# Kernel optimization log

Hardware: AMD Instinct MI355X
Metric: run time of the kernel (lower is better)

## Reference

```python
import jax, jax.numpy as jnp
import numpy as np

BS, HIST, H, W, NOBJ = 512, 3, 10, 10, 4
NSENT, TOK, DM = 3, 36, 768
EMB, FM, K, NL, ADIM = 256, 64, 2, 128, 5
LIN = FM * (H - (K - 1)) * (W - (K - 1))  # 64*9*9 = 5184
ATTN_SCALE = float(np.sqrt(EMB))  # 16.0


def setup_inputs() -> dict:
    key = jax.random.key(0)
    ks = jax.random.split(key, 24)
    g = lambda i, shape, s=0.02: jax.random.normal(ks[i], shape, dtype=jnp.float32) * s
    sprite_emb = g(0, (25, EMB), 1.0).at[0].set(0.0)  # padding_idx=0 -> zero row
    inp = {
        'state': jax.random.randint(ks[1], (BS, HIST, H, W, NOBJ), 0, 25, dtype=jnp.int32),
        'action': jax.random.randint(ks[2], (BS,), 0, ADIM, dtype=jnp.int32),
        'temb': jax.random.normal(ks[3], (BS, NSENT, TOK, DM), dtype=jnp.float32),
        'sprite_emb': sprite_emb,
        'conv_w': g(4, (K, K, HIST * EMB, FM)),  # HWIO
        'conv_b': g(5, (FM,)),
        'Wk': g(6, (DM, EMB)), 'bk': g(7, (EMB,)),
        'Wks': g(8, (DM, 1)), 'bks': g(9, (1,)),
        'Wv': g(10, (DM, EMB)), 'bv': g(11, (EMB,)),
        'Wvs': g(12, (DM, 1)), 'bvs': g(13, (1,)),
        'a1': g(14, (LIN, NL)), 'a1b': g(15, (NL,)),
        'a2': g(16, (NL, NL)), 'a2b': g(17, (NL,)),
        'a3': g(18, (NL, ADIM)), 'a3b': g(19, (ADIM,)),
        'v1': g(20, (LIN, NL)), 'v1b': g(21, (NL,)),
        'v2': g(22, (NL, NL)), 'v2b': g(23, (NL,)),
        'v3': jax.random.normal(jax.random.fold_in(key, 99), (NL, 1)) * 0.02,
        'v3b': jnp.zeros((1,), jnp.float32),
    }
    return inp


def _nonzero_mean(e):
    # e: [..., n, emb]; mean over rows that are nonzero (padding rows are all-zero)
    cnt = jnp.sum(jnp.sum(e, axis=-1) != 0, axis=-1, keepdims=True)
    return jnp.sum(e, axis=-2) / jnp.maximum(cnt, 1).astype(e.dtype)


def reference(state, action, temb, sprite_emb, conv_w, conv_b, Wk, bk, Wks, bks,
              Wv, bv, Wvs, bvs, a1, a1b, a2, a2b, a3, a3b, v1, v1b, v2, v2b, v3, v3b):
    lrelu = jax.nn.leaky_relu  # slope 0.01 matches torch default
    bs = state.shape[0]
    obj_state, avt_state = state[..., :-1], state[..., -1:]
    query = _nonzero_mean(sprite_emb[obj_state])   # [bs,hist,H,W,emb]
    avatar = _nonzero_mean(sprite_emb[avt_state])  # [bs,hist,H,W,emb]
    # text key/value: scaled token-softmax pooling over tokens (dim=2)
    k = (temb @ Wk + bk) * jax.nn.softmax(temb @ Wks + bks, axis=-2)
    k = jnp.sum(k, axis=2)                          # [bs,nsent,emb]
    v = (temb @ Wv + bv) * jax.nn.softmax(temb @ Wvs + bvs, axis=-2)
    v = jnp.sum(v, axis=2)                          # [bs,nsent,emb]
    # batch_attention
    q2 = query.reshape(bs, -1, EMB)                 # [bs, hist*H*W, emb]
    kq = jnp.einsum('bxe,bse->bxs', q2, k) / ATTN_SCALE
    wts = jax.nn.softmax(kq, axis=-1) * (kq != 0)
    wts = wts.reshape(bs, HIST, H, W, NSENT)
    # mean(weights[...,None]*value, dim=-2) == (w @ v) / nsent
    att = jnp.einsum('bthws,bse->bthwe', wts, v) / NSENT  # [bs,hist,H,W,emb]
    st = att.reshape(bs, H, W, -1)                  # fold hist into channels (768)
    av = avatar.reshape(bs, H, W, -1)
    st = (st + av) / 2.0                            # NHWC, C=768
    y = jax.lax.conv_general_dilated(st, conv_w, (1, 1), 'VALID',
                                     dimension_numbers=('NHWC', 'HWIO', 'NHWC')) + conv_b
    y = lrelu(y)                                    # [bs,9,9,64]
    y = jnp.transpose(y, (0, 3, 1, 2)).reshape(bs, -1)  # torch NCHW flatten order
    ha = lrelu(lrelu(y @ a1 + a1b) @ a2 + a2b)
    logits = ha @ a3 + a3b
    logp = jax.nn.log_softmax(logits, axis=-1)
    action_logprobs = jnp.take_along_axis(logp, action[:, None].astype(jnp.int32), axis=-1)[:, 0]
    entropy = -jnp.sum(jnp.exp(logp) * logp, axis=-1)
    hv = lrelu(lrelu(y @ v1 + v1b) @ v2 + v2b)
    state_value = (hv @ v3 + v3b)[:, 0]
    return action_logprobs, state_value, entropy
```

## Files before the change

kernel.cpp:

```cpp
#include <hip/hip_runtime.h>
#include <hip/hip_bf16.h>
#include <math.h>

constexpr int BS   = 512;
constexpr int NBS  = 1536;
constexpr int NPOS = 300;
constexpr int LIN  = 5184;
constexpr int KSPLIT = 9, KCH = 576;

typedef __attribute__((ext_vector_type(8))) short bf16x8;
typedef __attribute__((ext_vector_type(4))) float f32x4;

static __device__ __forceinline__ short f2bf(float f) {
    unsigned u = __float_as_uint(f);
    unsigned r = (u + 0x7FFFu + ((u >> 16) & 1u)) >> 16;
    return (short)r;
}
static __device__ __forceinline__ unsigned pk2(float a, float b) {
    return ((unsigned)(unsigned short)f2bf(a)) | (((unsigned)(unsigned short)f2bf(b)) << 16);
}
static __device__ __forceinline__ float bf2f_lo(unsigned u) { return __uint_as_float(u << 16); }
static __device__ __forceinline__ float bf2f_hi(unsigned u) { return __uint_as_float(u & 0xFFFF0000u); }

constexpr size_t OFF_RD   = 0;
constexpr size_t OFF_FL   = 19968;
constexpr size_t OFF_DT   = 20032;
constexpr size_t OFF_WCT  = 118336;
constexpr size_t OFF_PH   = 413248;
constexpr size_t OFF_AB   = 437824;
constexpr size_t OFF_SK   = 1101376;
constexpr size_t OFF_SV   = 1156672;
constexpr size_t OFF_SWK  = 1211968;
constexpr size_t OFF_SWV  = 1267264;
constexpr size_t OFF_XKH  = 1322560;
constexpr size_t OFF_XVH  = 1912384;
constexpr size_t OFF_VWH  = 2502208;
constexpr size_t OFF_YH   = 3092032;
constexpr size_t OFF_PART = 4419136;

__global__ __launch_bounds__(256) void kS_scores_prep(
    const float* __restrict__ temb, const float* __restrict__ Wks,
    const float* __restrict__ Wvs, const float* __restrict__ conv_w,
    const float* __restrict__ sprite, const float* __restrict__ Wk,
    const float* __restrict__ Wv, const float* __restrict__ bv,
    const float* __restrict__ a1, const float* __restrict__ v1,
    float* __restrict__ SK, float* __restrict__ SV,
    short* __restrict__ AB, short* __restrict__ PH, short* __restrict__ WCT,
    float* __restrict__ RD, int* __restrict__ FL)
{
    __shared__ float tile[64][65];
    int tid = threadIdx.x, bx = blockIdx.x;

    if (bx < 13824) {
        int wid = tid >> 6, lane = tid & 63;
        size_t r = (size_t)bx * 4 + wid;
        const float4* row = (const float4*)temb + r * 192;
        const float4* k4 = (const float4*)Wks;
        const float4* v4 = (const float4*)Wvs;
        float pk = 0.f, pv = 0.f;
        #pragma unroll
        for (int i = 0; i < 3; ++i) {
            int d4 = lane + 64 * i;
            float4 x = row[d4];
            float4 wk = k4[d4], wv = v4[d4];
            pk += x.x * wk.x + x.y * wk.y + x.z * wk.z + x.w * wk.w;
            pv += x.x * wv.x + x.y * wv.y + x.z * wv.z + x.w * wv.w;
        }
        #pragma unroll
        for (int off = 32; off; off >>= 1) {
            pk += __shfl_down(pk, off);
            pv += __shfl_down(pv, off);
        }
        if (lane == 0) { SK[r] = pk; SV[r] = pv; }
        return;
    }

    int id = bx - 13824;
    if (id < 324) {
        int kt = id % 81, nt = id / 81;
        const float* src = (nt < 2) ? a1 : v1;
        int col0 = (nt & 1) * 64;
        #pragma unroll
        for (int it = 0; it < 16; ++it) {
            int idx = it * 256 + tid; int ki = idx >> 6, ni = idx & 63;
            tile[ki][ni] = src[(size_t)(kt * 64 + ki) * 128 + col0 + ni];
        }
        __syncthreads();
        #pragma unroll
        for (int it = 0; it < 16; ++it) {
            int idx = it * 256 + tid; int ni = idx >> 6, ki = idx & 63;
            AB[(size_t)(nt * 64 + ni) * 5184 + kt * 64 + ki] = f2bf(tile[ki][ni]);
        }
    } else if (id < 399) {
        int g = (id - 324) * 256 + tid;
        if (g < 19200) {
            int o = g / 768, d = g - o * 768;
            const float* sp = sprite + o * 256;
            const float* wr = Wk + (size_t)d * 256;
            float s = 0.f;
            for (int c = 0; c < 256; ++c) s += sp[c] * wr[c];
            PH[(size_t)o * 768 + d] = f2bf(s);
        }
    } else if (id < 477) {
        int g = (id - 399) * 256 + tid;
        if (g < 19968) {
            int o = g / 768, n = g - o * 768;
            int tap = n >> 6, f = n & 63; int t4 = tap / 3, j = tap - t4 * 3;
            const float* sp = (o < 25) ? (sprite + o * 256) : bv;
            float s = 0.f;
            for (int e = 0; e < 256; ++e)
                s += sp[e] * conv_w[(size_t)(t4 * 768 + j * 256 + e) * 64 + f];
            RD[g] = s;
        }
    } else if (id < 621) {
        int wid2 = id - 477;
        int bm = (wid2 / 12) * 64, bn = (wid2 % 12) * 64;
        int p = bm >> 6; int t4 = p / 3, jj = p - t4 * 3;
        const float* cwb = conv_w + (size_t)(t4 * 768 + jj * 256) * 64;
        float* As = (float*)tile;
        float* Bs = (float*)tile + 2080;
        float acc[4][4];
        #pragma unroll
        for (int i = 0; i < 4; ++i)
            #pragma unroll
            for (int j = 0; j < 4; ++j) acc[i][j] = 0.f;
        int tm = tid >> 4, tn = tid & 15;
        for (int kc = 0; kc < 256; kc += 32) {
            #pragma unroll
            for (int it = 0; it < 8; ++it) {
                int idx = it * 256 + tid; int c = idx >> 6, f = idx & 63;
                As[c * 65 + f] = cwb[(size_t)(kc + c) * 64 + f];
            }
            #pragma unroll
            for (int it = 0; it < 8; ++it) {
                int idx = it * 256 + tid; int d = idx >> 5, c = idx & 31;
                Bs[c * 65 + d] = Wv[(size_t)(bn + d) * 256 + kc + c];
            }
            __syncthreads();
            for (int kk = 0; kk < 32; ++kk) {
                float a[4], b[4];
                #pragma unroll
                for (int i = 0; i < 4; ++i) a[i] = As[kk * 65 + tm * 4 + i];
                #pragma unroll
                for (int j = 0; j < 4; ++j) b[j] = Bs[kk * 65 + tn * 4 + j];
                #pragma unroll
                for (int i = 0; i < 4; ++i)
                    #pragma unroll
                    for (int j = 0; j < 4; ++j) acc[i][j] += a[i] * b[j];
            }
            __syncthreads();
        }
        #pragma unroll
        for (int i = 0; i < 4; ++i)
            #pragma unroll
            for (int j = 0; j < 4; ++j)
                WCT[(size_t)(bm + tm * 4 + i) * 768 + bn + tn * 4 + j] = f2bf(acc[i][j]);
    } else {
        if (tid < 25) {
            float s = 0.f;
            for (int c = 0; c < 256; ++c) s += sprite[tid * 256 + c];
            FL[tid] = (s != 0.0f) ? 1 : 0;
        }
    }
}

__global__ __launch_bounds__(512) void kW_weights(
    const float* __restrict__ SK, const float* __restrict__ SV,
    float* __restrict__ SWK, float* __restrict__ SWV)
{
    int w = threadIdx.x >> 6, lane = threadIdx.x & 63;
    int bs = blockIdx.x * 8 + w;
    {
        float s = (lane < 36) ? SK[(size_t)bs * 36 + lane] : -1e30f;
        float m = s;
        #pragma unroll
        for (int off = 32; off; off >>= 1) m = fmaxf(m, __shfl_xor(m, off));
        float e = (lane < 36) ? expf(s - m) : 0.f;
        float z = e;
        #pragma unroll
        for (int off = 32; off; off >>= 1) z += __shfl_xor(z, off);
        if (lane < 36) SWK[(size_t)bs * 36 + lane] = e / z;
    }
    {
        float s = (lane < 36) ? SV[(size_t)bs * 36 + lane] : -1e30f;
        float m = s;
        #pragma unroll
        for (int off = 32; off; off >>= 1) m = fmaxf(m, __shfl_xor(m, off));
        float e = (lane < 36) ? expf(s - m) : 0.f;
        float z = e;
        #pragma unroll
        for (int off = 32; off; off >>= 1) z += __shfl_xor(z, off);
        if (lane < 36) SWV[(size_t)bs * 36 + lane] = e / z;
    }
}

__global__ __launch_bounds__(192) void kX_sum(
    const float* __restrict__ temb, const float* __restrict__ SWK,
    const float* __restrict__ SWV, short* __restrict__ XKH, short* __restrict__ XVH)
{
    __shared__ float sw[72];
    int tid = threadIdx.x, bs = blockIdx.x;
    if (tid < 36) sw[tid] = SWK[(size_t)bs * 36 + tid];
    else if (tid >= 64 && tid < 100) sw[tid - 28] = SWV[(size_t)bs * 36 + tid - 64];
    __syncthreads();

    const float4* row4 = (const float4*)temb + (size_t)bs * 6912;
    float k0 = 0.f, k1 = 0.f, k2 = 0.f, k3 = 0.f;
    float v0 = 0.f, v1 = 0.f, v2 = 0.f, v3 = 0.f;
    #pragma unroll
    for (int b = 0; b < 3; ++b) {
        float4 xv[12];
        #pragma unroll
        for (int j = 0; j < 12; ++j) xv[j] = row4[(size_t)(b * 12 + j) * 192 + tid];
        #pragma unroll
        for (int j = 0; j < 12; ++j) {
            int t = b * 12 + j;
            float wk = sw[t], wv = sw[36 + t];
            k0 += wk * xv[j].x; k1 += wk * xv[j].y;
            k2 += wk * xv[j].z; k3 += wk * xv[j].w;
            v0 += wv * xv[j].x; v1 += wv * xv[j].y;
            v2 += wv * xv[j].z; v3 += wv * xv[j].w;
        }
    }
    uint2 hk = { pk2(k0, k1), pk2(k2, k3) };
    uint2 hv = { pk2(v0, v1), pk2(v2, v3) };
    ((uint2*)XKH)[(size_t)bs * 192 + tid] = hk;
    ((uint2*)XVH)[(size_t)bs * 192 + tid] = hv;
}

template<int BIAS, int OUTBF>
__global__ __launch_bounds__(256) void gemm_mfma(
    const short* __restrict__ A, const short* __restrict__ B,
    const float* __restrict__ bias, void* __restrict__ Cout,
    int K, int ldc, int klen, size_t czstride)
{
    __shared__ short As[64][40];
    __shared__ short Bs[64][40];
    int tid = threadIdx.x;
    int bm = blockIdx.x * 64, bn = blockIdx.y * 64;
    int wid = tid >> 6, lane = tid & 63;
    int wm = (wid >> 1) * 32, wn = (wid & 1) * 32;
    int l15 = lane & 15, lg = lane >> 4;

    f32x4 zero = {0.f, 0.f, 0.f, 0.f};
    f32x4 acc00 = zero, acc01 = zero, acc10 = zero, acc11 = zero;

    int srow = tid >> 2, kch = (tid & 3) * 8;
    const short* Ap = A + (size_t)(bm + srow) * K + kch + (size_t)blockIdx.z * klen;
    const short* Bp = B + (size_t)(bn + srow) * K + kch + (size_t)blockIdx.z * klen;

    for (int kt = 0; kt < klen; kt += 32) {
        bf16x8 aval = *(const bf16x8*)(Ap + kt);
        bf16x8 bval = *(const bf16x8*)(Bp + kt);
        *(bf16x8*)&As[srow][kch] = aval;
        *(bf16x8*)&Bs[srow][kch] = bval;
        __syncthreads();
        bf16x8 af0 = *(const bf16x8*)&As[wm + l15][lg * 8];
        bf16x8 af1 = *(const bf16x8*)&As[wm + 16 + l15][lg * 8];
        bf16x8 bg0 = *(const bf16x8*)&Bs[wn + l15][lg * 8];
        bf16x8 bg1 = *(const bf16x8*)&Bs[wn + 16 + l15][lg * 8];
        acc00 = __builtin_amdgcn_mfma_f32_16x16x32_bf16(af0, bg0, acc00, 0, 0, 0);
        acc01 = __builtin_amdgcn_mfma_f32_16x16x32_bf16(af0, bg1, acc01, 0, 0, 0);
        acc10 = __builtin_amdgcn_mfma_f32_16x16x32_bf16(af1, bg0, acc10, 0, 0, 0);
        acc11 = __builtin_amdgcn_mfma_f32_16x16x32_bf16(af1, bg1, acc11, 0, 0, 0);
        __syncthreads();
    }

    float* Cf = (float*)Cout + (size_t)blockIdx.z * czstride;
    short* Ch = (short*)Cout;
    #pragma unroll
    for (int i = 0; i < 2; ++i) {
        f32x4 arow0 = (i == 0) ? acc00 : acc10;
        f32x4 arow1 = (i == 0) ? acc01 : acc11;
        #pragma unroll
        for (int j = 0; j < 2; ++j) {
            f32x4 a = (j == 0) ? arow0 : arow1;
            int col = bn + wn + j * 16 + l15;
            float bb = BIAS ? bias[col] : 0.f;
            #pragma unroll
            for (int r = 0; r < 4; ++r) {
                int row = bm + wm + i * 16 + lg * 4 + r;
                float v = a[r] + bb;
                if (OUTBF) Ch[(size_t)row * ldc + col] = f2bf(v);
                else       Cf[(size_t)row * ldc + col] = v;
            }
        }
    }
}

__global__ __launch_bounds__(256) void k3_vwdt(
    const short* __restrict__ XVH, const short* __restrict__ WCT,
    const float* __restrict__ bvW2, short* __restrict__ VWH,
    const short* __restrict__ XKH, const short* __restrict__ PH,
    float* __restrict__ DT)
{
    __shared__ short As[64][40];
    __shared__ short Bs[64][40];
    int tid = threadIdx.x;
    bool isdt = (blockIdx.y == 12);
    const short* A = isdt ? XKH : XVH;
    const short* B = isdt ? PH  : WCT;
    int bm = blockIdx.x * 64, bn = isdt ? 0 : blockIdx.y * 64;
    int wid = tid >> 6, lane = tid & 63;
    int wm = (wid >> 1) * 32, wn = (wid & 1) * 32;
    int l15 = lane & 15, lg = lane >> 4;

    f32x4 zero = {0.f, 0.f, 0.f, 0.f};
    f32x4 acc00 = zero, acc01 = zero, acc10 = zero, acc11 = zero;

    int srow = tid >> 2, kch = (tid & 3) * 8;
    const short* Ap = A + (size_t)(bm + srow) * 768 + kch;
    const short* Bp = B + (size_t)(bn + srow) * 768 + kch;

    for (int kt = 0; kt < 768; kt += 32) {
        bf16x8 aval = *(const bf16x8*)(Ap + kt);
        bf16x8 bval = *(const bf16x8*)(Bp + kt);
        *(bf16x8*)&As[srow][kch] = aval;
        *(bf16x8*)&Bs[srow][kch] = bval;
        __syncthreads();
        bf16x8 af0 = *(const bf16x8*)&As[wm + l15][lg * 8];
        bf16x8 af1 = *(const bf16x8*)&As[wm + 16 + l15][lg * 8];
        bf16x8 bg0 = *(const bf16x8*)&Bs[wn + l15][lg * 8];
        bf16x8 bg1 = *(const bf16x8*)&Bs[wn + 16 + l15][lg * 8];
        acc00 = __builtin_amdgcn_mfma_f32_16x16x32_bf16(af0, bg0, acc00, 0, 0, 0);
        acc01 = __builtin_amdgcn_mfma_f32_16x16x32_bf16(af0, bg1, acc01, 0, 0, 0);
        acc10 = __builtin_amdgcn_mfma_f32_16x16x32_bf16(af1, bg0, acc10, 0, 0, 0);
        acc11 = __builtin_amdgcn_mfma_f32_16x16x32_bf16(af1, bg1, acc11, 0, 0, 0);
        __syncthreads();
    }

    #pragma unroll
    for (int i = 0; i < 2; ++i) {
        f32x4 arow0 = (i == 0) ? acc00 : acc10;
        f32x4 arow1 = (i == 0) ? acc01 : acc11;
        #pragma unroll
        for (int j = 0; j < 2; ++j) {
            f32x4 a = (j == 0) ? arow0 : arow1;
            int col = bn + wn + j * 16 + l15;
            #pragma unroll
            for (int r = 0; r < 4; ++r) {
                int row = bm + wm + i * 16 + lg * 4 + r;
                if (isdt) DT[(size_t)row * 64 + col] = a[r];
                else      VWH[(size_t)row * 768 + col] = f2bf(a[r] + bvW2[col]);
            }
        }
    }
}

__global__ __launch_bounds__(512) void k4_y(
    const int* __restrict__ state, const float* __restrict__ dt,
    const int* __restrict__ flags, const short* __restrict__ VWH,
    const float* __restrict__ rowdot, const float* __restrict__ conv_b,
    short* __restrict__ y)
{
    int b = blockIdx.x, tid = threadIdx.x;
    __shared__ float s_vW[3 * 768];
    __shared__ float s_w[3][NPOS + 4];
    __shared__ int   s_avt[NPOS + 4];
    __shared__ float s_y[81 * 65];

    const unsigned* vr = (const unsigned*)(VWH + (size_t)b * 3 * 768);
    for (int i = tid; i < 1152; i += 512) {
        unsigned u = vr[i];
        s_vW[2 * i]     = bf2f_lo(u);
        s_vW[2 * i + 1] = bf2f_hi(u);
    }

    for (int code = tid; code < NPOS; code += 512) {
        const int* st = state + ((size_t)b * NPOS + code) * 4;
        int o0 = st[0], o1 = st[1], o2 = st[2], avi = st[3];
        int cnt = flags[o0] + flags[o1] + flags[o2];
        s_avt[code] = avi;
        float w0 = 0.f, w1 = 0.f, w2 = 0.f;
        if (cnt > 0) {
            const float* d0 = dt + (size_t)b * 192;
            float inv = 1.0f / (16.0f * (float)cnt);
            float q0 = (d0[o0]       + d0[o1]       + d0[o2])       * inv;
            float q1 = (d0[64 + o0]  + d0[64 + o1]  + d0[64 + o2])  * inv;
            float q2 = (d0[128 + o0] + d0[128 + o1] + d0[128 + o2]) * inv;
            float m = fmaxf(q0, fmaxf(q1, q2));
            float e0 = expf(q0 - m), e1 = expf(q1 - m), e2 = expf(q2 - m);
            float is = 1.0f / (6.0f * (e0 + e1 + e2));
            w0 = e0 * is; w1 = e1 * is; w2 = e2 * is;
        }
        s_w[0][code] = w0; s_w[1][code] = w1; s_w[2][code] = w2;
    }
    __syncthreads();

    int f = tid & 63;
    float cb = conv_b[f];
    for (int p = tid >> 6; p < 81; p += 8) {
        int oh = p / 9, ow = p - oh * 9;
        float acc = cb;
        #pragma unroll
        for (int kh = 0; kh < 2; ++kh)
        #pragma unroll
        for (int kw = 0; kw < 2; ++kw) {
            int bc = 3 * ((oh + kh) * 10 + (ow + kw));
            int tbase = ((kh * 2 + kw) * 3) * 64 + f;
            #pragma unroll
            for (int j = 0; j < 3; ++j) {
                int code = bc + j;
                int tf = tbase + j * 64;
                acc += s_w[0][code] * s_vW[tf]
                     + s_w[1][code] * s_vW[768 + tf]
                     + s_w[2][code] * s_vW[2 * 768 + tf];
                acc += 0.5f * rowdot[(size_t)s_avt[code] * 768 + tf];
            }
        }
        acc = acc > 0.f ? acc : 0.01f * acc;
        s_y[p * 65 + f] = acc;
    }
    __syncthreads();
    for (int i = tid; i < LIN; i += 512) {
        int ff = i / 81, pp = i - ff * 81;
        y[(size_t)b * LIN + i] = f2bf(s_y[pp * 65 + ff]);
    }
}

__global__ __launch_bounds__(128) void k6_heads(
    const float* __restrict__ PART, const float* __restrict__ a1b,
    const float* __restrict__ v1b, const int* __restrict__ action,
    const float* __restrict__ a2, const float* __restrict__ a2b,
    const float* __restrict__ a3, const float* __restrict__ a3b,
    const float* __restrict__ v2, const float* __restrict__ v2b,
    const float* __restrict__ v3, const float* __restrict__ v3b,
    float* __restrict__ out)
{
    int b = blockIdx.x, tid = threadIdx.x;
    __shared__ float h1a[128], h1v[128], h2a[128], red[128];
    __shared__ float lg[5];
    float sa0 = a1b[tid], sv0 = v1b[tid];
    const float* pb = PART + (size_t)b * 256;
    for (int z = 0; z < KSPLIT; ++z) {
        sa0 += pb[(size_t)z * (BS * 256) + tid];
        sv0 += pb[(size_t)z * (BS * 256) + 128 + tid];
    }
    h1a[tid] = sa0 > 0.f ? sa0 : 0.01f * sa0;
    h1v[tid] = sv0 > 0.f ? sv0 : 0.01f * sv0;
    __syncthreads();
    float sa = a2b[tid], sv = v2b[tid];
    for (int k = 0; k < 128; ++k) {
        sa += h1a[k] * a2[k * 128 + tid];
        sv += h1v[k] * v2[k * 128 + tid];
    }
    sa = sa > 0.f ? sa : 0.01f * sa;
    sv = sv > 0.f ? sv : 0.01f * sv;
    h2a[tid] = sa;
    red[tid] = sv * v3[tid];
    __syncthreads();
    for (int s = 64; s > 0; s >>= 1) {
        if (tid < s) red[tid] += red[tid + s];
        __syncthreads();
    }
    if (tid < 5) {
        float l = a3b[tid];
        for (int k = 0; k < 128; ++k) l += h2a[k] * a3[k * 5 + tid];
        lg[tid] = l;
    }
    __syncthreads();
    if (tid == 0) {
        float m = lg[0];
        for (int j2 = 1; j2 < 5; ++j2) m = fmaxf(m, lg[j2]);
        float se = 0.f;
        for (int j2 = 0; j2 < 5; ++j2) se += expf(lg[j2] - m);
        float lse = m + logf(se);
        int act = action[b];
        float ent = 0.f;
        for (int j2 = 0; j2 < 5; ++j2) {
            float lp = lg[j2] - lse;
            ent -= expf(lp) * lp;
        }
        out[b]        = lg[act] - lse;
        out[512 + b]  = red[0] + v3b[0];
        out[1024 + b] = ent;
    }
}

extern "C" void kernel_launch(void* const* d_in, const int* in_sizes, int n_in,
                              void* d_out, int out_size, void* d_ws, size_t ws_size,
                              hipStream_t stream)
{
    const int*   state  = (const int*)d_in[0];
    const int*   action = (const int*)d_in[1];
    const float* temb   = (const float*)d_in[2];
    const float* sprite = (const float*)d_in[3];
    const float* conv_w = (const float*)d_in[4];
    const float* conv_b = (const float*)d_in[5];
    const float* Wk     = (const float*)d_in[6];
    const float* Wks    = (const float*)d_in[8];
    const float* Wv     = (const float*)d_in[10];
    const float* bv     = (const float*)d_in[11];
    const float* Wvs    = (const float*)d_in[12];
    const float* a1     = (const float*)d_in[14];
    const float* a1b    = (const float*)d_in[15];
    const float* a2     = (const float*)d_in[16];
    const float* a2b    = (const float*)d_in[17];
    const float* a3     = (const float*)d_in[18];
    const float* a3b    = (const float*)d_in[19];
    const float* v1     = (const float*)d_in[20];
    const float* v1b    = (const float*)d_in[21];
    const float* v2     = (const float*)d_in[22];
    const float* v2b    = (const float*)d_in[23];
    const float* v3     = (const float*)d_in[24];
    const float* v3b    = (const float*)d_in[25];
    (void)in_sizes; (void)n_in; (void)out_size; (void)ws_size;

    float* ws  = (float*)d_ws;
    float* RD  = ws + OFF_RD;
    float* bvW2= RD + 25 * 768;
    int*   FL  = (int*)(ws + OFF_FL);
    float* DT  = ws + OFF_DT;
    short* WCT = (short*)(ws + OFF_WCT);
    short* PH  = (short*)(ws + OFF_PH);
    short* AB  = (short*)(ws + OFF_AB);
    float* SK  = ws + OFF_SK;
    float* SV  = ws + OFF_SV;
    float* SWK = ws + OFF_SWK;
    float* SWV = ws + OFF_SWV;
    short* XKH = (short*)(ws + OFF_XKH);
    short* XVH = (short*)(ws + OFF_XVH);
    short* VWH = (short*)(ws + OFF_VWH);
    short* YH  = (short*)(ws + OFF_YH);
    float* PART= ws + OFF_PART;
    float* out = (float*)d_out;

    kS_scores_prep<<<13824 + 622, 256, 0, stream>>>(
        temb, Wks, Wvs, conv_w, sprite, Wk, Wv, bv, a1, v1,
        SK, SV, AB, PH, WCT, RD, FL);
    kW_weights<<<192, 512, 0, stream>>>(SK, SV, SWK, SWV);
    kX_sum<<<NBS, 192, 0, stream>>>(temb, SWK, SWV, XKH, XVH);
    k3_vwdt<<<dim3(24,13,1),256,0,stream>>>(XVH, WCT, bvW2, VWH, XKH, PH, DT);
    k4_y<<<BS, 512, 0, stream>>>(state, DT, FL, VWH, RD, conv_b, YH);
    gemm_mfma<0,0><<<dim3(8,4,KSPLIT),256,0,stream>>>(YH, AB, nullptr, PART, 5184, 256, KCH, (size_t)BS*256);
    k6_heads<<<BS, 128, 0, stream>>>(PART, a1b, v1b, action, a2, a2b, a3, a3b,
                                     v2, v2b, v3, v3b, out);
}
```

Before: 137.7 us.

## Fuse token scoring, softmax and weighted pooling into one temb pass

```diff
diff --git a/kernel.cpp b/kernel.cpp
--- a/kernel.cpp
+++ b/kernel.cpp
@@ -28,81 +28,162 @@
 constexpr size_t OFF_WCT  = 118336;
 constexpr size_t OFF_PH   = 413248;
 constexpr size_t OFF_AB   = 437824;
-constexpr size_t OFF_SK   = 1101376;
-constexpr size_t OFF_SV   = 1156672;
-constexpr size_t OFF_SWK  = 1211968;
-constexpr size_t OFF_SWV  = 1267264;
-constexpr size_t OFF_XKH  = 1322560;
-constexpr size_t OFF_XVH  = 1912384;
-constexpr size_t OFF_VWH  = 2502208;
-constexpr size_t OFF_YH   = 3092032;
-constexpr size_t OFF_PART = 4419136;
-
-__global__ __launch_bounds__(256) void kS_scores_prep(
+constexpr size_t OFF_XKH  = 1101376;
+constexpr size_t OFF_XVH  = 1691200;
+constexpr size_t OFF_VWH  = 2281024;
+constexpr size_t OFF_YH   = 2870848;
+constexpr size_t OFF_PART = 4197952;
+
+#define DOT4(a,b) ((a).x*(b).x + (a).y*(b).y + (a).z*(b).z + (a).w*(b).w)
+#define WRED(v) { v += __shfl_down(v,32); v += __shfl_down(v,16); v += __shfl_down(v,8); \
+                  v += __shfl_down(v,4);  v += __shfl_down(v,2);  v += __shfl_down(v,1); }
+
+__global__ __launch_bounds__(576) void kT_temb_prep(
     const float* __restrict__ temb, const float* __restrict__ Wks,
     const float* __restrict__ Wvs, const float* __restrict__ conv_w,
     const float* __restrict__ sprite, const float* __restrict__ Wk,
     const float* __restrict__ Wv, const float* __restrict__ bv,
     const float* __restrict__ a1, const float* __restrict__ v1,
-    float* __restrict__ SK, float* __restrict__ SV,
+    short* __restrict__ XKH, short* __restrict__ XVH,
     short* __restrict__ AB, short* __restrict__ PH, short* __restrict__ WCT,
     float* __restrict__ RD, int* __restrict__ FL)
 {
-    __shared__ float tile[64][65];
+    __shared__ float spart[9][26];
+    __shared__ float swt[80];
+    __shared__ float big[4608];
     int tid = threadIdx.x, bx = blockIdx.x;
 
-    if (bx < 13824) {
-        int wid = tid >> 6, lane = tid & 63;
-        size_t r = (size_t)bx * 4 + wid;
-        const float4* row = (const float4*)temb + r * 192;
-        const float4* k4 = (const float4*)Wks;
-        const float4* v4 = (const float4*)Wvs;
-        float pk = 0.f, pv = 0.f;
-        #pragma unroll
-        for (int i = 0; i < 3; ++i) {
-            int d4 = lane + 64 * i;
-            float4 x = row[d4];
-            float4 wk = k4[d4], wv = v4[d4];
-            pk += x.x * wk.x + x.y * wk.y + x.z * wk.z + x.w * wk.w;
-            pv += x.x * wv.x + x.y * wv.y + x.z * wv.z + x.w * wv.w;
-        }
-        #pragma unroll
-        for (int off = 32; off; off >>= 1) {
-            pk += __shfl_down(pk, off);
-            pv += __shfl_down(pv, off);
-        }
-        if (lane == 0) { SK[r] = pk; SV[r] = pv; }
+    if (bx < NBS) {
+        int bs = bx;
+        int w = tid >> 6, lane = tid & 63;
+        int g = tid / 192, c = tid - g * 192;
+        const float4* row4 = (const float4*)temb + (size_t)bs * 6912 + (size_t)g * 2304 + c;
+
+        float4 x0  = row4[0];
+        float4 x1  = row4[192];
+        float4 x2  = row4[384];
+        float4 x3  = row4[576];
+        float4 x4  = row4[768];
+        float4 x5  = row4[960];
+        float4 x6  = row4[1152];
+        float4 x7  = row4[1344];
+        float4 x8  = row4[1536];
+        float4 x9  = row4[1728];
+        float4 x10 = row4[1920];
+        float4 x11 = row4[2112];
+        float4 wk = ((const float4*)Wks)[c];
+        float4 wv = ((const float4*)Wvs)[c];
+
+        float pk0 = DOT4(x0,wk),  pv0 = DOT4(x0,wv);
+        float pk1 = DOT4(x1,wk),  pv1 = DOT4(x1,wv);
+        float pk2_ = DOT4(x2,wk), pv2 = DOT4(x2,wv);
+        float pk3 = DOT4(x3,wk),  pv3 = DOT4(x3,wv);
+        float pk4 = DOT4(x4,wk),  pv4 = DOT4(x4,wv);
+        float pk5 = DOT4(x5,wk),  pv5 = DOT4(x5,wv);
+        float pk6 = DOT4(x6,wk),  pv6 = DOT4(x6,wv);
+        float pk7 = DOT4(x7,wk),  pv7 = DOT4(x7,wv);
+        float pk8 = DOT4(x8,wk),  pv8 = DOT4(x8,wv);
+        float pk9 = DOT4(x9,wk),  pv9 = DOT4(x9,wv);
+        float pk10 = DOT4(x10,wk), pv10 = DOT4(x10,wv);
+        float pk11 = DOT4(x11,wk), pv11 = DOT4(x11,wv);
+
+        WRED(pk0)  WRED(pk1)  WRED(pk2_) WRED(pk3)  WRED(pk4)  WRED(pk5)
+        WRED(pk6)  WRED(pk7)  WRED(pk8)  WRED(pk9)  WRED(pk10) WRED(pk11)
+        WRED(pv0)  WRED(pv1)  WRED(pv2)  WRED(pv3)  WRED(pv4)  WRED(pv5)
+        WRED(pv6)  WRED(pv7)  WRED(pv8)  WRED(pv9)  WRED(pv10) WRED(pv11)
+
+        if (lane == 0) {
+            spart[w][0] = pk0;   spart[w][1] = pk1;   spart[w][2] = pk2_;
+            spart[w][3] = pk3;   spart[w][4] = pk4;   spart[w][5] = pk5;
+            spart[w][6] = pk6;   spart[w][7] = pk7;   spart[w][8] = pk8;
+            spart[w][9] = pk9;   spart[w][10] = pk10; spart[w][11] = pk11;
+            spart[w][12] = pv0;  spart[w][13] = pv1;  spart[w][14] = pv2;
+            spart[w][15] = pv3;  spart[w][16] = pv4;  spart[w][17] = pv5;
+            spart[w][18] = pv6;  spart[w][19] = pv7;  spart[w][20] = pv8;
+            spart[w][21] = pv9;  spart[w][22] = pv10; spart[w][23] = pv11;
+        }
+        __syncthreads();
+
+        if (w == 0) {
+            float sk = -INFINITY, sv = -INFINITY;
+            if (lane < 36) {
+                int t = lane, gg = t / 12, j = t - gg * 12;
+                sk = spart[3*gg][j]    + spart[3*gg+1][j]    + spart[3*gg+2][j];
+                sv = spart[3*gg][12+j] + spart[3*gg+1][12+j] + spart[3*gg+2][12+j];
+            }
+            float mk = sk, mv = sv;
+            #pragma unroll
+            for (int off = 32; off; off >>= 1) {
+                mk = fmaxf(mk, __shfl_xor(mk, off));
+                mv = fmaxf(mv, __shfl_xor(mv, off));
+            }
+            float ek = (lane < 36) ? expf(sk - mk) : 0.f;
+            float ev = (lane < 36) ? expf(sv - mv) : 0.f;
+            float zk = ek, zv = ev;
+            #pragma unroll
+            for (int off = 32; off; off >>= 1) {
+                zk += __shfl_xor(zk, off);
+                zv += __shfl_xor(zv, off);
+            }
+            if (lane < 36) { swt[lane] = ek / zk; swt[40 + lane] = ev / zv; }
+        }
+        __syncthreads();
+
+        float4 ak = {0.f,0.f,0.f,0.f}, av = {0.f,0.f,0.f,0.f};
+        int wb = 12 * g;
+        #define ACCJ(J, XJ) { float a_ = swt[wb + J], b_ = swt[40 + wb + J]; \
+            ak.x += a_*XJ.x; ak.y += a_*XJ.y; ak.z += a_*XJ.z; ak.w += a_*XJ.w; \
+            av.x += b_*XJ.x; av.y += b_*XJ.y; av.z += b_*XJ.z; av.w += b_*XJ.w; }
+        ACCJ(0,x0) ACCJ(1,x1) ACCJ(2,x2) ACCJ(3,x3) ACCJ(4,x4) ACCJ(5,x5)
+        ACCJ(6,x6) ACCJ(7,x7) ACCJ(8,x8) ACCJ(9,x9) ACCJ(10,x10) ACCJ(11,x11)
+        #undef ACCJ
+
+        float4* red = (float4*)big;
+        red[g * 192 + c] = ak;
+        red[576 + g * 192 + c] = av;
+        __syncthreads();
+        if (tid < 192) {
+            float4 a0 = red[tid], a1_ = red[192 + tid], a2 = red[384 + tid];
+            float4 b0 = red[576 + tid], b1 = red[768 + tid], b2 = red[960 + tid];
+            float kx = a0.x + a1_.x + a2.x, ky = a0.y + a1_.y + a2.y;
+            float kz = a0.z + a1_.z + a2.z, kw = a0.w + a1_.w + a2.w;
+            float vx = b0.x + b1.x + b2.x, vy = b0.y + b1.y + b2.y;
+            float vz = b0.z + b1.z + b2.z, vw = b0.w + b1.w + b2.w;
+            uint2 hk = { pk2(kx, ky), pk2(kz, kw) };
+            uint2 hv = { pk2(vx, vy), pk2(vz, vw) };
+            ((uint2*)XKH)[(size_t)bs * 192 + tid] = hk;
+            ((uint2*)XVH)[(size_t)bs * 192 + tid] = hv;
+        }
         return;
     }
 
-    int id = bx - 13824;
+    int id = bx - NBS;
     if (id < 324) {
+        float (*tile)[65] = (float(*)[65])big;
         int kt = id % 81, nt = id / 81;
         const float* src = (nt < 2) ? a1 : v1;
         int col0 = (nt & 1) * 64;
-        #pragma unroll
-        for (int it = 0; it < 16; ++it) {
-            int idx = it * 256 + tid; int ki = idx >> 6, ni = idx & 63;
+        for (int idx = tid; idx < 4096; idx += 576) {
+            int ki = idx >> 6, ni = idx & 63;
             tile[ki][ni] = src[(size_t)(kt * 64 + ki) * 128 + col0 + ni];
         }
         __syncthreads();
-        #pragma unroll
-        for (int it = 0; it < 16; ++it) {
-            int idx = it * 256 + tid; int ni = idx >> 6, ki = idx & 63;
+        for (int idx = tid; idx < 4096; idx += 576) {
+            int ni = idx >> 6, ki = idx & 63;
             AB[(size_t)(nt * 64 + ni) * 5184 + kt * 64 + ki] = f2bf(tile[ki][ni]);
         }
-    } else if (id < 399) {
-        int g = (id - 324) * 256 + tid;
+    } else if (id < 358) {
+        int g = (id - 324) * 576 + tid;
         if (g < 19200) {
             int o = g / 768, d = g - o * 768;
             const float* sp = sprite + o * 256;
             const float* wr = Wk + (size_t)d * 256;
             float s = 0.f;
-            for (int c = 0; c < 256; ++c) s += sp[c] * wr[c];
+            for (int cc = 0; cc < 256; ++cc) s += sp[cc] * wr[cc];
             PH[(size_t)o * 768 + d] = f2bf(s);
         }
-    } else if (id < 477) {
-        int g = (id - 399) * 256 + tid;
+    } else if (id < 393) {
+        int g = (id - 358) * 576 + tid;
         if (g < 19968) {
             int o = g / 768, n = g - o * 768;
             int tap = n >> 6, f = n & 63; int t4 = tap / 3, j = tap - t4 * 3;
@@ -112,178 +193,56 @@
                 s += sp[e] * conv_w[(size_t)(t4 * 768 + j * 256 + e) * 64 + f];
             RD[g] = s;
         }
-    } else if (id < 621) {
-        int wid2 = id - 477;
+    } else if (id < 537) {
+        int wid2 = id - 393;
         int bm = (wid2 / 12) * 64, bn = (wid2 % 12) * 64;
         int p = bm >> 6; int t4 = p / 3, jj = p - t4 * 3;
         const float* cwb = conv_w + (size_t)(t4 * 768 + jj * 256) * 64;
-        float* As = (float*)tile;
-        float* Bs = (float*)tile + 2080;
+        float* As = big;
+        float* Bs = big + 2080;
         float acc[4][4];
         #pragma unroll
         for (int i = 0; i < 4; ++i)
             #pragma unroll
             for (int j = 0; j < 4; ++j) acc[i][j] = 0.f;
-        int tm = tid >> 4, tn = tid & 15;
+        int tm = (tid & 255) >> 4, tn = tid & 15;
         for (int kc = 0; kc < 256; kc += 32) {
-            #pragma unroll
-            for (int it = 0; it < 8; ++it) {
-                int idx = it * 256 + tid; int c = idx >> 6, f = idx & 63;
-                As[c * 65 + f] = cwb[(size_t)(kc + c) * 64 + f];
-            }
-            #pragma unroll
-            for (int it = 0; it < 8; ++it) {
-                int idx = it * 256 + tid; int d = idx >> 5, c = idx & 31;
-                Bs[c * 65 + d] = Wv[(size_t)(bn + d) * 256 + kc + c];
+            for (int idx = tid; idx < 2048; idx += 576) {
+                int cc = idx >> 6, f = idx & 63;
+                As[cc * 65 + f] = cwb[(size_t)(kc + cc) * 64 + f];
+            }
+            for (int idx = tid; idx < 2048; idx += 576) {
+                int d = idx >> 5, cc = idx & 31;
+                Bs[cc * 65 + d] = Wv[(size_t)(bn + d) * 256 + kc + cc];
             }
             __syncthreads();
-            for (int kk = 0; kk < 32; ++kk) {
-                float a[4], b[4];
+            if (tid < 256) {
+                for (int kk = 0; kk < 32; ++kk) {
+                    float a[4], b[4];
+                    #pragma unroll
+                    for (int i = 0; i < 4; ++i) a[i] = As[kk * 65 + tm * 4 + i];
+                    #pragma unroll
+                    for (int j = 0; j < 4; ++j) b[j] = Bs[kk * 65 + tn * 4 + j];
+                    #pragma unroll
+                    for (int i = 0; i < 4; ++i)
+                        #pragma unroll
+                        for (int j = 0; j < 4; ++j) acc[i][j] += a[i] * b[j];
+                }
+            }
+            __syncthreads();
+        }
+        if (tid < 256) {
+            #pragma unroll
+            for (int i = 0; i < 4; ++i)
                 #pragma unroll
-                for (int i = 0; i < 4; ++i) a[i] = As[kk * 65 + tm * 4 + i];
-                #pragma unroll
-                for (int j = 0; j < 4; ++j) b[j] = Bs[kk * 65 + tn * 4 + j];
-                #pragma unroll
-                for (int i = 0; i < 4; ++i)
-                    #pragma unroll
-                    for (int j = 0; j < 4; ++j) acc[i][j] += a[i] * b[j];
-            }
-            __syncthreads();
-        }
-        #pragma unroll
-        for (int i = 0; i < 4; ++i)
-            #pragma unroll
-            for (int j = 0; j < 4; ++j)
-                WCT[(size_t)(bm + tm * 4 + i) * 768 + bn + tn * 4 + j] = f2bf(acc[i][j]);
+                for (int j = 0; j < 4; ++j)
+                    WCT[(size_t)(bm + tm * 4 + i) * 768 + bn + tn * 4 + j] = f2bf(acc[i][j]);
+        }
     } else {
         if (tid < 25) {
             float s = 0.f;
-            for (int c = 0; c < 256; ++c) s += sprite[tid * 256 + c];
+            for (int cc = 0; cc < 256; ++cc) s += sprite[tid * 256 + cc];
             FL[tid] = (s != 0.0f) ? 1 : 0;
-        }
-    }
-}
-
-__global__ __launch_bounds__(512) void kW_weights(
-    const float* __restrict__ SK, const float* __restrict__ SV,
-    float* __restrict__ SWK, float* __restrict__ SWV)
-{
-    int w = threadIdx.x >> 6, lane = threadIdx.x & 63;
-    int bs = blockIdx.x * 8 + w;
-    {
-        float s = (lane < 36) ? SK[(size_t)bs * 36 + lane] : -1e30f;
-        float m = s;
-        #pragma unroll
-        for (int off = 32; off; off >>= 1) m = fmaxf(m, __shfl_xor(m, off));
-        float e = (lane < 36) ? expf(s - m) : 0.f;
-        float z = e;
-        #pragma unroll
-        for (int off = 32; off; off >>= 1) z += __shfl_xor(z, off);
-        if (lane < 36) SWK[(size_t)bs * 36 + lane] = e / z;
-    }
-    {
-        float s = (lane < 36) ? SV[(size_t)bs * 36 + lane] : -1e30f;
-        float m = s;
-        #pragma unroll
-        for (int off = 32; off; off >>= 1) m = fmaxf(m, __shfl_xor(m, off));
-        float e = (lane < 36) ? expf(s - m) : 0.f;
-        float z = e;
-        #pragma unroll
-        for (int off = 32; off; off >>= 1) z += __shfl_xor(z, off);
-        if (lane < 36) SWV[(size_t)bs * 36 + lane] = e / z;
-    }
-}
-
-__global__ __launch_bounds__(192) void kX_sum(
-    const float* __restrict__ temb, const float* __restrict__ SWK,
-    const float* __restrict__ SWV, short* __restrict__ XKH, short* __restrict__ XVH)
-{
-    __shared__ float sw[72];
-    int tid = threadIdx.x, bs = blockIdx.x;
-    if (tid < 36) sw[tid] = SWK[(size_t)bs * 36 + tid];
-    else if (tid >= 64 && tid < 100) sw[tid - 28] = SWV[(size_t)bs * 36 + tid - 64];
-    __syncthreads();
-
-    const float4* row4 = (const float4*)temb + (size_t)bs * 6912;
-    float k0 = 0.f, k1 = 0.f, k2 = 0.f, k3 = 0.f;
-    float v0 = 0.f, v1 = 0.f, v2 = 0.f, v3 = 0.f;
-    #pragma unroll
-    for (int b = 0; b < 3; ++b) {
-        float4 xv[12];
-        #pragma unroll
-        for (int j = 0; j < 12; ++j) xv[j] = row4[(size_t)(b * 12 + j) * 192 + tid];
-        #pragma unroll
-        for (int j = 0; j < 12; ++j) {
-            int t = b * 12 + j;
-            float wk = sw[t], wv = sw[36 + t];
-            k0 += wk * xv[j].x; k1 += wk * xv[j].y;
-            k2 += wk * xv[j].z; k3 += wk * xv[j].w;
-            v0 += wv * xv[j].x; v1 += wv * xv[j].y;
-            v2 += wv * xv[j].z; v3 += wv * xv[j].w;
-        }
-    }
-    uint2 hk = { pk2(k0, k1), pk2(k2, k3) };
-    uint2 hv = { pk2(v0, v1), pk2(v2, v3) };
-    ((uint2*)XKH)[(size_t)bs * 192 + tid] = hk;
-    ((uint2*)XVH)[(size_t)bs * 192 + tid] = hv;
-}
-
-template<int BIAS, int OUTBF>
-__global__ __launch_bounds__(256) void gemm_mfma(
-    const short* __restrict__ A, const short* __restrict__ B,
-    const float* __restrict__ bias, void* __restrict__ Cout,
-    int K, int ldc, int klen, size_t czstride)
-{
-    __shared__ short As[64][40];
-    __shared__ short Bs[64][40];
-    int tid = threadIdx.x;
-    int bm = blockIdx.x * 64, bn = blockIdx.y * 64;
-    int wid = tid >> 6, lane = tid & 63;
-    int wm = (wid >> 1) * 32, wn = (wid & 1) * 32;
-    int l15 = lane & 15, lg = lane >> 4;
-
-    f32x4 zero = {0.f, 0.f, 0.f, 0.f};
-    f32x4 acc00 = zero, acc01 = zero, acc10 = zero, acc11 = zero;
-
-    int srow = tid >> 2, kch = (tid & 3) * 8;
-    const short* Ap = A + (size_t)(bm + srow) * K + kch + (size_t)blockIdx.z * klen;
-    const short* Bp = B + (size_t)(bn + srow) * K + kch + (size_t)blockIdx.z * klen;
-
-    for (int kt = 0; kt < klen; kt += 32) {
-        bf16x8 aval = *(const bf16x8*)(Ap + kt);
-        bf16x8 bval = *(const bf16x8*)(Bp + kt);
-        *(bf16x8*)&As[srow][kch] = aval;
-        *(bf16x8*)&Bs[srow][kch] = bval;
-        __syncthreads();
-        bf16x8 af0 = *(const bf16x8*)&As[wm + l15][lg * 8];
-        bf16x8 af1 = *(const bf16x8*)&As[wm + 16 + l15][lg * 8];
-        bf16x8 bg0 = *(const bf16x8*)&Bs[wn + l15][lg * 8];
-        bf16x8 bg1 = *(const bf16x8*)&Bs[wn + 16 + l15][lg * 8];
-        acc00 = __builtin_amdgcn_mfma_f32_16x16x32_bf16(af0, bg0, acc00, 0, 0, 0);
-        acc01 = __builtin_amdgcn_mfma_f32_16x16x32_bf16(af0, bg1, acc01, 0, 0, 0);
-        acc10 = __builtin_amdgcn_mfma_f32_16x16x32_bf16(af1, bg0, acc10, 0, 0, 0);
-        acc11 = __builtin_amdgcn_mfma_f32_16x16x32_bf16(af1, bg1, acc11, 0, 0, 0);
-        __syncthreads();
-    }
-
-    float* Cf = (float*)Cout + (size_t)blockIdx.z * czstride;
-    short* Ch = (short*)Cout;
-    #pragma unroll
-    for (int i = 0; i < 2; ++i) {
-        f32x4 arow0 = (i == 0) ? acc00 : acc10;
-        f32x4 arow1 = (i == 0) ? acc01 : acc11;
-        #pragma unroll
-        for (int j = 0; j < 2; ++j) {
-            f32x4 a = (j == 0) ? arow0 : arow1;
-            int col = bn + wn + j * 16 + l15;
-            float bb = BIAS ? bias[col] : 0.f;
-            #pragma unroll
-            for (int r = 0; r < 4; ++r) {
-                int row = bm + wm + i * 16 + lg * 4 + r;
-                float v = a[r] + bb;
-                if (OUTBF) Ch[(size_t)row * ldc + col] = f2bf(v);
-                else       Cf[(size_t)row * ldc + col] = v;
-            }
         }
     }
 }
@@ -342,6 +301,66 @@
                 int row = bm + wm + i * 16 + lg * 4 + r;
                 if (isdt) DT[(size_t)row * 64 + col] = a[r];
                 else      VWH[(size_t)row * 768 + col] = f2bf(a[r] + bvW2[col]);
+            }
+        }
+    }
+}
+
+template<int BIAS, int OUTBF>
+__global__ __launch_bounds__(256) void gemm_mfma(
+    const short* __restrict__ A, const short* __restrict__ B,
+    const float* __restrict__ bias, void* __restrict__ Cout,
+    int K, int ldc, int klen, size_t czstride)
+{
+    __shared__ short As[64][40];
+    __shared__ short Bs[64][40];
+    int tid = threadIdx.x;
+    int bm = blockIdx.x * 64, bn = blockIdx.y * 64;
+    int wid = tid >> 6, lane = tid & 63;
+    int wm = (wid >> 1) * 32, wn = (wid & 1) * 32;
+    int l15 = lane & 15, lg = lane >> 4;
+
+    f32x4 zero = {0.f, 0.f, 0.f, 0.f};
+    f32x4 acc00 = zero, acc01 = zero, acc10 = zero, acc11 = zero;
+
+    int srow = tid >> 2, kch = (tid & 3) * 8;
+    const short* Ap = A + (size_t)(bm + srow) * K + kch + (size_t)blockIdx.z * klen;
+    const short* Bp = B + (size_t)(bn + srow) * K + kch + (size_t)blockIdx.z * klen;
+
+    for (int kt = 0; kt < klen; kt += 32) {
+        bf16x8 aval = *(const bf16x8*)(Ap + kt);
+        bf16x8 bval = *(const bf16x8*)(Bp + kt);
+        *(bf16x8*)&As[srow][kch] = aval;
+        *(bf16x8*)&Bs[srow][kch] = bval;
+        __syncthreads();
+        bf16x8 af0 = *(const bf16x8*)&As[wm + l15][lg * 8];
+        bf16x8 af1 = *(const bf16x8*)&As[wm + 16 + l15][lg * 8];
+        bf16x8 bg0 = *(const bf16x8*)&Bs[wn + l15][lg * 8];
+        bf16x8 bg1 = *(const bf16x8*)&Bs[wn + 16 + l15][lg * 8];
+        acc00 = __builtin_amdgcn_mfma_f32_16x16x32_bf16(af0, bg0, acc00, 0, 0, 0);
+        acc01 = __builtin_amdgcn_mfma_f32_16x16x32_bf16(af0, bg1, acc01, 0, 0, 0);
+        acc10 = __builtin_amdgcn_mfma_f32_16x16x32_bf16(af1, bg0, acc10, 0, 0, 0);
+        acc11 = __builtin_amdgcn_mfma_f32_16x16x32_bf16(af1, bg1, acc11, 0, 0, 0);
+        __syncthreads();
+    }
+
+    float* Cf = (float*)Cout + (size_t)blockIdx.z * czstride;
+    short* Ch = (short*)Cout;
+    #pragma unroll
+    for (int i = 0; i < 2; ++i) {
+        f32x4 arow0 = (i == 0) ? acc00 : acc10;
+        f32x4 arow1 = (i == 0) ? acc01 : acc11;
+        #pragma unroll
+        for (int j = 0; j < 2; ++j) {
+            f32x4 a = (j == 0) ? arow0 : arow1;
+            int col = bn + wn + j * 16 + l15;
+            float bb = BIAS ? bias[col] : 0.f;
+            #pragma unroll
+            for (int r = 0; r < 4; ++r) {
+                int row = bm + wm + i * 16 + lg * 4 + r;
+                float v = a[r] + bb;
+                if (OUTBF) Ch[(size_t)row * ldc + col] = f2bf(v);
+                else       Cf[(size_t)row * ldc + col] = v;
             }
         }
     }
@@ -514,10 +533,6 @@
     short* WCT = (short*)(ws + OFF_WCT);
     short* PH  = (short*)(ws + OFF_PH);
     short* AB  = (short*)(ws + OFF_AB);
-    float* SK  = ws + OFF_SK;
-    float* SV  = ws + OFF_SV;
-    float* SWK = ws + OFF_SWK;
-    float* SWV = ws + OFF_SWV;
     short* XKH = (short*)(ws + OFF_XKH);
     short* XVH = (short*)(ws + OFF_XVH);
     short* VWH = (short*)(ws + OFF_VWH);
@@ -525,11 +540,9 @@
     float* PART= ws + OFF_PART;
     float* out = (float*)d_out;
 
-    kS_scores_prep<<<13824 + 622, 256, 0, stream>>>(
+    kT_temb_prep<<<NBS + 538, 576, 0, stream>>>(
         temb, Wks, Wvs, conv_w, sprite, Wk, Wv, bv, a1, v1,
-        SK, SV, AB, PH, WCT, RD, FL);
-    kW_weights<<<192, 512, 0, stream>>>(SK, SV, SWK, SWV);
-    kX_sum<<<NBS, 192, 0, stream>>>(temb, SWK, SWV, XKH, XVH);
+        XKH, XVH, AB, PH, WCT, RD, FL);
     k3_vwdt<<<dim3(24,13,1),256,0,stream>>>(XVH, WCT, bvW2, VWH, XKH, PH, DT);
     k4_y<<<BS, 512, 0, stream>>>(state, DT, FL, VWH, RD, conv_b, YH);
     gemm_mfma<0,0><<<dim3(8,4,KSPLIT),256,0,stream>>>(YH, AB, nullptr, PART, 5184, 256, KCH, (size_t)BS*256);
```

Measured after the change: 129.2 us. 6.2% less time.
